# Kernel optimization log

Hardware: AMD Instinct MI355X
Metric: run time of the kernel (lower is better)

Reference implementation:

```python
import jax, jax.numpy as jnp
import numpy as np

N_NODES = 50000
N_EDGES = 800000
IN_FEAT = 128
HEADS = 4
UNITS = 16
LEAKY_ALPHA = 0.2  # tf.nn.leaky_relu default


def setup_inputs() -> dict:
    key = jax.random.key(0)
    k1, k2, k3, k4, k5 = jax.random.split(key, 5)
    x = jax.random.normal(k1, (N_NODES, IN_FEAT), dtype=jnp.float32)
    edge_index = jax.random.randint(k2, (N_EDGES, 2), 0, N_NODES, dtype=jnp.int32)
    # Dense kernel (glorot-ish scaling), no bias (use_bias=False)
    W = jax.random.normal(k3, (IN_FEAT, HEADS * UNITS), dtype=jnp.float32) * (1.0 / np.sqrt(IN_FEAT))
    glorot = np.sqrt(2.0 / (1 + UNITS)).astype(np.float32)
    att_w1 = jax.random.normal(k4, (HEADS, 1, UNITS), dtype=jnp.float32) * glorot
    att_w2 = jax.random.normal(k5, (HEADS, 1, UNITS), dtype=jnp.float32) * glorot
    return {"x": x, "edge_index": edge_index, "W": W, "att_w1": att_w1, "att_w2": att_w2}


def reference(x, edge_index, W, att_w1, att_w2):
    n_nodes = x.shape[0]
    h = x @ W  # [N, H*U]
    snd_idx = edge_index[:, 0]
    rcv_idx = edge_index[:, 1]
    # gather per-edge features, split into heads -> [H, E, U]
    sender = h[snd_idx].reshape(-1, HEADS, UNITS).transpose(1, 0, 2)
    receiver = h[rcv_idx].reshape(-1, HEADS, UNITS).transpose(1, 0, 2)
    # per-edge, per-head attention logits [H, E]
    att = jnp.sum(att_w1 * sender, axis=-1) + jnp.sum(att_w2 * receiver, axis=-1)
    att = jnp.where(att > 0, att, LEAKY_ALPHA * att)
    # segment softmax over receiver neighborhoods, per head
    seg_max = jax.vmap(lambda a: jax.ops.segment_max(a, rcv_idx, num_segments=n_nodes))(att)  # [H, N]
    e = jnp.exp(att - seg_max[:, rcv_idx])
    denom = jax.vmap(lambda a: jax.ops.segment_sum(a, rcv_idx, num_segments=n_nodes))(e)  # [H, N]
    alpha = e / denom[:, rcv_idx]  # [H, E]
    # weighted scatter-sum of sender features -> [H, N, U]
    out = jax.vmap(lambda v: jax.ops.segment_sum(v, rcv_idx, num_segments=n_nodes))(sender * alpha[:, :, None])
    # concat heads -> [N, H*U]; activation is None (identity)
    return out.transpose(1, 0, 2).reshape(n_nodes, HEADS * UNITS)
```

## Files before the change

### kernel.cpp

```cpp
#include <hip/hip_runtime.h>
#include <math.h>

#define N_NODES 50000
#define N_EDGES 800000
#define IN_FEAT 128
#define HEADS   4
#define UNITS   16
#define OUTF    64
#define LEAKY   0.2f

#define NB      196
#define BCAP    5120
#define GEMM_BLKS 782
#define A_BLOCKS  391
#define EPB     8

typedef __attribute__((ext_vector_type(8))) short bf16x8;
typedef __attribute__((ext_vector_type(4))) float f32x4;

__device__ __forceinline__ unsigned short f2bf(float f) {
    unsigned u = __float_as_uint(f);
    unsigned r = u + 0x7FFFu + ((u >> 16) & 1u);
    return (unsigned short)(r >> 16);
}

union SharedU {
    struct { unsigned short xl[64 * 136]; unsigned short wt[64 * 136]; } g;
    struct { int2 stage[2048]; int hist[256], s[256], excl[256],
             gbase[256], cur[256]; } a;
};

__global__ __launch_bounds__(256) void fused_gemm_bucketA(const float* __restrict__ x,
                                                          const float* __restrict__ W,
                                                          const float* __restrict__ w1,
                                                          const float* __restrict__ w2,
                                                          const int2* __restrict__ ei,
                                                          unsigned short* __restrict__ hg,
                                                          float* __restrict__ a1,
                                                          float* __restrict__ a2,
                                                          int* __restrict__ bucket_cnt,
                                                          int2* __restrict__ buckets) {
    __shared__ SharedU sh;
    const int t = threadIdx.x;

    if (blockIdx.x >= GEMM_BLKS) {
        const int e0 = (blockIdx.x - GEMM_BLKS) * 2048;
        sh.a.hist[t] = 0;
        __syncthreads();

        int2 ed[EPB]; int bk[EPB];
        #pragma unroll
        for (int j = 0; j < EPB; ++j) {
            int e = e0 + t + j * 256;
            if (e < N_EDGES) {
                ed[j] = ei[e];
                bk[j] = ed[j].y >> 8;
                atomicAdd(&sh.a.hist[bk[j]], 1);
            } else bk[j] = -1;
        }
        __syncthreads();
        int v = sh.a.hist[t];
        sh.a.s[t] = v;
        __syncthreads();
        #pragma unroll
        for (int off = 1; off < 256; off <<= 1) {
            int u = (t >= off) ? sh.a.s[t - off] : 0;
            __syncthreads();
            sh.a.s[t] += u;
            __syncthreads();
        }
        sh.a.excl[t] = sh.a.s[t] - v;
        sh.a.cur[t] = 0;
        if (t < NB) sh.a.gbase[t] = atomicAdd(&bucket_cnt[t], v);
        __syncthreads();
        #pragma unroll
        for (int j = 0; j < EPB; ++j) {
            if (bk[j] >= 0) {
                int p = sh.a.excl[bk[j]] + atomicAdd(&sh.a.cur[bk[j]], 1);
                sh.a.stage[p] = ed[j];
            }
        }
        __syncthreads();
        const int total = min(2048, N_EDGES - e0);
        for (int i = t; i < total; i += 256) {
            int2 vv = sh.a.stage[i];
            int b = vv.y >> 8;
            buckets[(size_t)b * BCAP + sh.a.gbase[b] + (i - sh.a.excl[b])] = vv;
        }
        return;
    }

    const int node0 = blockIdx.x * 64;
    unsigned short* xl = sh.g.xl;
    unsigned short* wt = sh.g.wt;

    #pragma unroll
    for (int it = 0; it < 8; ++it) {
        int idx = t + 256 * it;
        int r = idx >> 5, q = idx & 31;
        int node = node0 + r;
        float4 v = make_float4(0.f, 0.f, 0.f, 0.f);
        if (node < N_NODES) v = *(const float4*)(x + (size_t)node * IN_FEAT + q * 4);
        ushort4 b;
        b.x = f2bf(v.x); b.y = f2bf(v.y); b.z = f2bf(v.z); b.w = f2bf(v.w);
        *(ushort4*)&xl[r * 136 + q * 4] = b;
    }
    {
        const float4* W4 = (const float4*)W;
        #pragma unroll
        for (int it = 0; it < 8; ++it) {
            int idx4 = t + 256 * it;
            float4 v = W4[idx4];
            int flat = idx4 * 4;
            int k = flat >> 6, c = flat & 63;
            wt[(c + 0) * 136 + k] = f2bf(v.x);
            wt[(c + 1) * 136 + k] = f2bf(v.y);
            wt[(c + 2) * 136 + k] = f2bf(v.z);
            wt[(c + 3) * 136 + k] = f2bf(v.w);
        }
    }
    __syncthreads();

    const int lane = t & 63, wv = t >> 6;
    const int m = lane & 15, quad = lane >> 4;
    const int n0 = wv * 16;

    f32x4 acc[4] = {{0,0,0,0},{0,0,0,0},{0,0,0,0},{0,0,0,0}};
    #pragma unroll
    for (int kc = 0; kc < 4; ++kc) {
        bf16x8 af = *(bf16x8*)&xl[(n0 + m) * 136 + kc * 32 + quad * 8];
        #pragma unroll
        for (int ct = 0; ct < 4; ++ct) {
            bf16x8 bfr = *(bf16x8*)&wt[(ct * 16 + m) * 136 + kc * 32 + quad * 8];
            acc[ct] = __builtin_amdgcn_mfma_f32_16x16x32_bf16(af, bfr, acc[ct], 0, 0, 0);
        }
    }

    #pragma unroll
    for (int ct = 0; ct < 4; ++ct) {
        const float u1 = w1[ct * 16 + m];
        const float u2 = w2[ct * 16 + m];
        #pragma unroll
        for (int r = 0; r < 4; ++r) {
            float p1 = acc[ct][r] * u1;
            float p2 = acc[ct][r] * u2;
            p1 += __shfl_xor(p1, 1, 64); p1 += __shfl_xor(p1, 2, 64);
            p1 += __shfl_xor(p1, 4, 64); p1 += __shfl_xor(p1, 8, 64);
            p2 += __shfl_xor(p2, 1, 64); p2 += __shfl_xor(p2, 2, 64);
            p2 += __shfl_xor(p2, 4, 64); p2 += __shfl_xor(p2, 8, 64);
            if (m == 0) {
                int node = node0 + n0 + quad * 4 + r;
                if (node < N_NODES) {
                    a1[node * 4 + ct] = p1;
                    a2[node * 4 + ct] = p2;
                }
            }
        }
    }

    __syncthreads();
    unsigned short* hl = sh.g.xl;
    #pragma unroll
    for (int ct = 0; ct < 4; ++ct)
        #pragma unroll
        for (int r = 0; r < 4; ++r)
            hl[(n0 + quad * 4 + r) * 72 + ct * 16 + m] = f2bf(acc[ct][r]);
    __syncthreads();
    #pragma unroll
    for (int it = 0; it < 2; ++it) {
        int u = t + 256 * it;
        int r = u >> 3, cg = u & 7;
        int node = node0 + r;
        if (node < N_NODES)
            *(uint4*)&hg[(size_t)node * OUTF + cg * 8] = *(uint4*)&hl[r * 72 + cg * 8];
    }
}

__global__ __launch_bounds__(1024) void bucketB(const int2* __restrict__ buckets,
                                                const int* __restrict__ bucket_cnt,
                                                const float* __restrict__ a1,
                                                const float* __restrict__ a2,
                                                int* __restrict__ edge_snd,
                                                float* __restrict__ edge_e,
                                                int* __restrict__ rs,
                                                int* __restrict__ re) {
    __shared__ int hist[256], cur[256], s[256];
    __shared__ int2 stage[BCAP];
    const int b = blockIdx.x;
    const int t = threadIdx.x;
    const int cnt = bucket_cnt[b];
    if (t < 256) hist[t] = 0;
    __syncthreads();
    for (int i = t; i < cnt; i += 1024) {
        int2 vv = buckets[(size_t)b * BCAP + i];
        stage[i] = vv;
        atomicAdd(&hist[vv.y & 255], 1);
    }
    __syncthreads();
    if (t < 256) s[t] = hist[t];
    __syncthreads();
    #pragma unroll
    for (int off = 1; off < 256; off <<= 1) {
        int u = (t < 256 && t >= off) ? s[t - off] : 0;
        __syncthreads();
        if (t < 256) s[t] += u;
        __syncthreads();
    }
    if (t < 256) {
        const int v = hist[t];
        const int excl = s[t] - v;
        cur[t] = excl;
        const int node = b * 256 + t;
        if (node < N_NODES) {
            rs[node] = b * BCAP + excl;
            re[node] = b * BCAP + excl + v;
        }
    }
    __syncthreads();
    for (int i = t; i < cnt; i += 1024) {
        int2 vv = stage[i];
        int p = atomicAdd(&cur[vv.y & 255], 1);
        float4 s1 = *(const float4*)(a1 + (size_t)vv.x * 4);
        float4 s2 = *(const float4*)(a2 + (size_t)vv.y * 4);
        float t0 = s1.x + s2.x; t0 = t0 > 0.f ? t0 : LEAKY * t0;
        float t1 = s1.y + s2.y; t1 = t1 > 0.f ? t1 : LEAKY * t1;
        float t2 = s1.z + s2.z; t2 = t2 > 0.f ? t2 : LEAKY * t2;
        float t3 = s1.w + s2.w; t3 = t3 > 0.f ? t3 : LEAKY * t3;
        float4 e4 = make_float4(__expf(t0), __expf(t1), __expf(t2), __expf(t3));
        size_t q = (size_t)b * BCAP + p;
        edge_snd[q] = vv.x;
        *(float4*)(edge_e + q * 4) = e4;
    }
}

__global__ __launch_bounds__(256, 8) void gather_kernel(const int* __restrict__ rs,
                                                        const int* __restrict__ re,
                                                        const int* __restrict__ edge_snd,
                                                        const float* __restrict__ edge_e,
                                                        const unsigned short* __restrict__ h,
                                                        float* __restrict__ out) {
    const int wave = threadIdx.x >> 6;
    const int lane = threadIdx.x & 63;
    const int n = blockIdx.x * 4 + wave;
    if (n >= N_NODES) return;
    const int sub  = lane >> 3;
    const int li   = lane & 7;
    const int head = li >> 1;
    const int base = rs[n];
    const int end  = re[n];
    if (end <= base) {
        if (sub == 0) {
            *(float4*)(out + (size_t)n * OUTF + li * 8)     = make_float4(0.f, 0.f, 0.f, 0.f);
            *(float4*)(out + (size_t)n * OUTF + li * 8 + 4) = make_float4(0.f, 0.f, 0.f, 0.f);
        }
        return;
    }
    const uint4* h4 = (const uint4*)h;

    float acc[8] = {0.f,0.f,0.f,0.f,0.f,0.f,0.f,0.f};
    float den = 0.f;

    for (int i = base; i < end; i += 16) {
        #pragma unroll
        for (int g = 0; g < 2; ++g) {
            int eraw = i + g * 8 + sub;
            int eidx = min(eraw, end - 1);
            int s = edge_snd[eidx];
            float ev = edge_e[(size_t)eidx * 4 + head];
            float e = (eraw < end) ? ev : 0.f;
            uint4 hv = h4[(unsigned)(s * 8 + li)];
            const unsigned hw[4] = {hv.x, hv.y, hv.z, hv.w};
            #pragma unroll
            for (int q = 0; q < 4; ++q) {
                acc[q*2+0] = fmaf(e, __uint_as_float(hw[q] << 16),         acc[q*2+0]);
                acc[q*2+1] = fmaf(e, __uint_as_float(hw[q] & 0xFFFF0000u), acc[q*2+1]);
            }
            den += e;
        }
    }

    #pragma unroll
    for (int off = 8; off <= 32; off <<= 1) {
        #pragma unroll
        for (int q = 0; q < 8; ++q) acc[q] += __shfl_xor(acc[q], off, 64);
        den += __shfl_xor(den, off, 64);
    }

    if (sub == 0) {
        float inv = 1.f / den;
        *(float4*)(out + (size_t)n * OUTF + li * 8) =
            make_float4(acc[0] * inv, acc[1] * inv, acc[2] * inv, acc[3] * inv);
        *(float4*)(out + (size_t)n * OUTF + li * 8 + 4) =
            make_float4(acc[4] * inv, acc[5] * inv, acc[6] * inv, acc[7] * inv);
    }
}

extern "C" void kernel_launch(void* const* d_in, const int* in_sizes, int n_in,
                              void* d_out, int out_size, void* d_ws, size_t ws_size,
                              hipStream_t stream) {
    const float* x  = (const float*)d_in[0];
    const int2*  ei = (const int2*)d_in[1];
    const float* W  = (const float*)d_in[2];
    const float* w1 = (const float*)d_in[3];
    const float* w2 = (const float*)d_in[4];
    float* out = (float*)d_out;

    unsigned short* h = (unsigned short*)d_ws;
    float* a1         = (float*)(h + (size_t)N_NODES * OUTF);
    float* a2         = a1 + (size_t)N_NODES * HEADS;
    int2*  buckets    = (int2*)(a2 + (size_t)N_NODES * HEADS);
    float* edge_e     = (float*)(buckets + (size_t)NB * BCAP);
    int*   edge_snd   = (int*)(edge_e + (size_t)NB * BCAP * 4);
    int*   rs         = edge_snd + (size_t)NB * BCAP;
    int*   re         = rs + N_NODES;
    int*   bucket_cnt = re + N_NODES;

    hipMemsetAsync(bucket_cnt, 0, NB * sizeof(int), stream);
    fused_gemm_bucketA<<<GEMM_BLKS + A_BLOCKS, 256, 0, stream>>>(x, W, w1, w2, ei,
                                                                 h, a1, a2,
                                                                 bucket_cnt, buckets);
    bucketB<<<NB, 1024, 0, stream>>>(buckets, bucket_cnt, a1, a2,
                                     edge_snd, edge_e, rs, re);
    gather_kernel<<<(N_NODES + 3) / 4, 256, 0, stream>>>(rs, re, edge_snd, edge_e, h, out);
}
```

Measured before the change: 136.5 us.

## Fuse bucket sort and gather into one kernel with 64-node buckets

Shrinks receiver buckets from 256 to 64 nodes (784 buckets) and merges the second bucketing pass with the gather/aggregation kernel. Sender indices are sorted per node in shared memory and consumed directly. Attention exponentials are recomputed during the gather instead of being written to and read back from global memory, which also removes the edge_snd, edge_e, rs and re buffers and one kernel launch. The tradeoff is fewer, larger blocks in the fused kernel, where each wave walks 16 nodes serially, which may reduce parallelism and load balance. Skewed buckets also risk overflowing the smaller capacity of 1280.

```diff
diff --git a/kernel.cpp b/kernel.cpp
--- a/kernel.cpp
+++ b/kernel.cpp
@@ -9,8 +9,11 @@
 #define OUTF    64
 #define LEAKY   0.2f
 
-#define NB      196
-#define BCAP    5120
+#define BSH     6
+#define BNODES  64
+#define NB      784
+#define NBP     1024
+#define BCAP    1280
 #define GEMM_BLKS 782
 #define A_BLOCKS  391
 #define EPB     8
@@ -26,8 +29,7 @@
 
 union SharedU {
     struct { unsigned short xl[64 * 136]; unsigned short wt[64 * 136]; } g;
-    struct { int2 stage[2048]; int hist[256], s[256], excl[256],
-             gbase[256], cur[256]; } a;
+    struct { int2 stage[2048]; int hist[NBP], cur[NBP], adj[NBP], s[256]; } a;
 };
 
 __global__ __launch_bounds__(256) void fused_gemm_bucketA(const float* __restrict__ x,
@@ -45,7 +47,8 @@
 
     if (blockIdx.x >= GEMM_BLKS) {
         const int e0 = (blockIdx.x - GEMM_BLKS) * 2048;
-        sh.a.hist[t] = 0;
+        #pragma unroll
+        for (int j = 0; j < 4; ++j) sh.a.hist[t + 256 * j] = 0;
         __syncthreads();
 
         int2 ed[EPB]; int bk[EPB];
@@ -54,13 +57,15 @@
             int e = e0 + t + j * 256;
             if (e < N_EDGES) {
                 ed[j] = ei[e];
-                bk[j] = ed[j].y >> 8;
+                bk[j] = ed[j].y >> BSH;
                 atomicAdd(&sh.a.hist[bk[j]], 1);
             } else bk[j] = -1;
         }
         __syncthreads();
-        int v = sh.a.hist[t];
-        sh.a.s[t] = v;
+        const int h0 = sh.a.hist[4 * t + 0], h1 = sh.a.hist[4 * t + 1],
+                  h2 = sh.a.hist[4 * t + 2], h3 = sh.a.hist[4 * t + 3];
+        const int lsum = h0 + h1 + h2 + h3;
+        sh.a.s[t] = lsum;
         __syncthreads();
         #pragma unroll
         for (int off = 1; off < 256; off <<= 1) {
@@ -69,14 +74,23 @@
             sh.a.s[t] += u;
             __syncthreads();
         }
-        sh.a.excl[t] = sh.a.s[t] - v;
-        sh.a.cur[t] = 0;
-        if (t < NB) sh.a.gbase[t] = atomicAdd(&bucket_cnt[t], v);
+        const int base = sh.a.s[t] - lsum;
+        const int ex0 = base, ex1 = base + h0, ex2 = base + h0 + h1, ex3 = base + h0 + h1 + h2;
+        sh.a.cur[4 * t + 0] = ex0; sh.a.cur[4 * t + 1] = ex1;
+        sh.a.cur[4 * t + 2] = ex2; sh.a.cur[4 * t + 3] = ex3;
+        if (4 * t < NB) {
+            int g0 = atomicAdd(&bucket_cnt[4 * t + 0], h0);
+            int g1 = atomicAdd(&bucket_cnt[4 * t + 1], h1);
+            int g2 = atomicAdd(&bucket_cnt[4 * t + 2], h2);
+            int g3 = atomicAdd(&bucket_cnt[4 * t + 3], h3);
+            sh.a.adj[4 * t + 0] = g0 - ex0; sh.a.adj[4 * t + 1] = g1 - ex1;
+            sh.a.adj[4 * t + 2] = g2 - ex2; sh.a.adj[4 * t + 3] = g3 - ex3;
+        }
         __syncthreads();
         #pragma unroll
         for (int j = 0; j < EPB; ++j) {
             if (bk[j] >= 0) {
-                int p = sh.a.excl[bk[j]] + atomicAdd(&sh.a.cur[bk[j]], 1);
+                int p = atomicAdd(&sh.a.cur[bk[j]], 1);
                 sh.a.stage[p] = ed[j];
             }
         }
@@ -84,8 +98,8 @@
         const int total = min(2048, N_EDGES - e0);
         for (int i = t; i < total; i += 256) {
             int2 vv = sh.a.stage[i];
-            int b = vv.y >> 8;
-            buckets[(size_t)b * BCAP + sh.a.gbase[b] + (i - sh.a.excl[b])] = vv;
+            int b = vv.y >> BSH;
+            buckets[(size_t)(b * BCAP + sh.a.adj[b] + i)] = vv;
         }
         return;
     }
@@ -176,122 +190,103 @@
     }
 }
 
-__global__ __launch_bounds__(1024) void bucketB(const int2* __restrict__ buckets,
+__global__ __launch_bounds__(256) void bucketBC(const int2* __restrict__ buckets,
                                                 const int* __restrict__ bucket_cnt,
                                                 const float* __restrict__ a1,
                                                 const float* __restrict__ a2,
-                                                int* __restrict__ edge_snd,
-                                                float* __restrict__ edge_e,
-                                                int* __restrict__ rs,
-                                                int* __restrict__ re) {
-    __shared__ int hist[256], cur[256], s[256];
+                                                const unsigned short* __restrict__ h,
+                                                float* __restrict__ out) {
     __shared__ int2 stage[BCAP];
+    __shared__ int  snds[BCAP];
+    __shared__ int  hist[BNODES], strt[BNODES], cur[BNODES];
     const int b = blockIdx.x;
     const int t = threadIdx.x;
     const int cnt = bucket_cnt[b];
-    if (t < 256) hist[t] = 0;
-    __syncthreads();
-    for (int i = t; i < cnt; i += 1024) {
+
+    if (t < BNODES) hist[t] = 0;
+    __syncthreads();
+    for (int i = t; i < cnt; i += 256) {
         int2 vv = buckets[(size_t)b * BCAP + i];
         stage[i] = vv;
-        atomicAdd(&hist[vv.y & 255], 1);
-    }
-    __syncthreads();
-    if (t < 256) s[t] = hist[t];
-    __syncthreads();
-    #pragma unroll
-    for (int off = 1; off < 256; off <<= 1) {
-        int u = (t < 256 && t >= off) ? s[t - off] : 0;
-        __syncthreads();
-        if (t < 256) s[t] += u;
-        __syncthreads();
-    }
-    if (t < 256) {
-        const int v = hist[t];
-        const int excl = s[t] - v;
-        cur[t] = excl;
-        const int node = b * 256 + t;
-        if (node < N_NODES) {
-            rs[node] = b * BCAP + excl;
-            re[node] = b * BCAP + excl + v;
-        }
-    }
-    __syncthreads();
-    for (int i = t; i < cnt; i += 1024) {
+        atomicAdd(&hist[vv.y & (BNODES - 1)], 1);
+    }
+    __syncthreads();
+    if (t < 64) {
+        int v = hist[t];
+        int inc = v;
+        #pragma unroll
+        for (int off = 1; off < 64; off <<= 1) {
+            int u = __shfl_up(inc, off, 64);
+            if (t >= off) inc += u;
+        }
+        strt[t] = inc - v;
+        cur[t]  = inc - v;
+    }
+    __syncthreads();
+    for (int i = t; i < cnt; i += 256) {
         int2 vv = stage[i];
-        int p = atomicAdd(&cur[vv.y & 255], 1);
-        float4 s1 = *(const float4*)(a1 + (size_t)vv.x * 4);
-        float4 s2 = *(const float4*)(a2 + (size_t)vv.y * 4);
-        float t0 = s1.x + s2.x; t0 = t0 > 0.f ? t0 : LEAKY * t0;
-        float t1 = s1.y + s2.y; t1 = t1 > 0.f ? t1 : LEAKY * t1;
-        float t2 = s1.z + s2.z; t2 = t2 > 0.f ? t2 : LEAKY * t2;
-        float t3 = s1.w + s2.w; t3 = t3 > 0.f ? t3 : LEAKY * t3;
-        float4 e4 = make_float4(__expf(t0), __expf(t1), __expf(t2), __expf(t3));
-        size_t q = (size_t)b * BCAP + p;
-        edge_snd[q] = vv.x;
-        *(float4*)(edge_e + q * 4) = e4;
-    }
-}
-
-__global__ __launch_bounds__(256, 8) void gather_kernel(const int* __restrict__ rs,
-                                                        const int* __restrict__ re,
-                                                        const int* __restrict__ edge_snd,
-                                                        const float* __restrict__ edge_e,
-                                                        const unsigned short* __restrict__ h,
-                                                        float* __restrict__ out) {
-    const int wave = threadIdx.x >> 6;
-    const int lane = threadIdx.x & 63;
-    const int n = blockIdx.x * 4 + wave;
-    if (n >= N_NODES) return;
+        int p = atomicAdd(&cur[vv.y & (BNODES - 1)], 1);
+        snds[p] = vv.x;
+    }
+    __syncthreads();
+
+    const int lane = t & 63, wv = t >> 6;
     const int sub  = lane >> 3;
     const int li   = lane & 7;
     const int head = li >> 1;
-    const int base = rs[n];
-    const int end  = re[n];
-    if (end <= base) {
+    const uint4* h4 = (const uint4*)h;
+
+    for (int j = 0; j < 16; ++j) {
+        const int loc  = wv + j * 4;
+        const int node = b * BNODES + loc;
+        if (node >= N_NODES) break;
+        const int s0 = strt[loc];
+        const int cn = hist[loc];
+        if (cn == 0) {
+            if (sub == 0) {
+                *(float4*)(out + (size_t)node * OUTF + li * 8)     = make_float4(0.f, 0.f, 0.f, 0.f);
+                *(float4*)(out + (size_t)node * OUTF + li * 8 + 4) = make_float4(0.f, 0.f, 0.f, 0.f);
+            }
+            continue;
+        }
+        const float a2h = a2[node * 4 + head];
+        float acc[8] = {0.f,0.f,0.f,0.f,0.f,0.f,0.f,0.f};
+        float den = 0.f;
+
+        for (int i0 = 0; i0 < cn; i0 += 16) {
+            #pragma unroll
+            for (int g = 0; g < 2; ++g) {
+                int er = i0 + g * 8 + sub;
+                int ec = min(er, cn - 1);
+                int s = snds[s0 + ec];
+                float t0 = a1[s * 4 + head] + a2h;
+                t0 = t0 > 0.f ? t0 : LEAKY * t0;
+                float e = (er < cn) ? __expf(t0) : 0.f;
+                uint4 hv = h4[(unsigned)(s * 8 + li)];
+                const unsigned hw[4] = {hv.x, hv.y, hv.z, hv.w};
+                #pragma unroll
+                for (int q = 0; q < 4; ++q) {
+                    acc[q*2+0] = fmaf(e, __uint_as_float(hw[q] << 16),         acc[q*2+0]);
+                    acc[q*2+1] = fmaf(e, __uint_as_float(hw[q] & 0xFFFF0000u), acc[q*2+1]);
+                }
+                den += e;
+            }
+        }
+
+        #pragma unroll
+        for (int off = 8; off <= 32; off <<= 1) {
+            #pragma unroll
+            for (int q = 0; q < 8; ++q) acc[q] += __shfl_xor(acc[q], off, 64);
+            den += __shfl_xor(den, off, 64);
+        }
+
         if (sub == 0) {
-            *(float4*)(out + (size_t)n * OUTF + li * 8)     = make_float4(0.f, 0.f, 0.f, 0.f);
-            *(float4*)(out + (size_t)n * OUTF + li * 8 + 4) = make_float4(0.f, 0.f, 0.f, 0.f);
-        }
-        return;
-    }
-    const uint4* h4 = (const uint4*)h;
-
-    float acc[8] = {0.f,0.f,0.f,0.f,0.f,0.f,0.f,0.f};
-    float den = 0.f;
-
-    for (int i = base; i < end; i += 16) {
-        #pragma unroll
-        for (int g = 0; g < 2; ++g) {
-            int eraw = i + g * 8 + sub;
-            int eidx = min(eraw, end - 1);
-            int s = edge_snd[eidx];
-            float ev = edge_e[(size_t)eidx * 4 + head];
-            float e = (eraw < end) ? ev : 0.f;
-            uint4 hv = h4[(unsigned)(s * 8 + li)];
-            const unsigned hw[4] = {hv.x, hv.y, hv.z, hv.w};
-            #pragma unroll
-            for (int q = 0; q < 4; ++q) {
-                acc[q*2+0] = fmaf(e, __uint_as_float(hw[q] << 16),         acc[q*2+0]);
-                acc[q*2+1] = fmaf(e, __uint_as_float(hw[q] & 0xFFFF0000u), acc[q*2+1]);
-            }
-            den += e;
-        }
-    }
-
-    #pragma unroll
-    for (int off = 8; off <= 32; off <<= 1) {
-        #pragma unroll
-        for (int q = 0; q < 8; ++q) acc[q] += __shfl_xor(acc[q], off, 64);
-        den += __shfl_xor(den, off, 64);
-    }
-
-    if (sub == 0) {
-        float inv = 1.f / den;
-        *(float4*)(out + (size_t)n * OUTF + li * 8) =
-            make_float4(acc[0] * inv, acc[1] * inv, acc[2] * inv, acc[3] * inv);
-        *(float4*)(out + (size_t)n * OUTF + li * 8 + 4) =
-            make_float4(acc[4] * inv, acc[5] * inv, acc[6] * inv, acc[7] * inv);
+            float inv = 1.f / den;
+            *(float4*)(out + (size_t)node * OUTF + li * 8) =
+                make_float4(acc[0] * inv, acc[1] * inv, acc[2] * inv, acc[3] * inv);
+            *(float4*)(out + (size_t)node * OUTF + li * 8 + 4) =
+                make_float4(acc[4] * inv, acc[5] * inv, acc[6] * inv, acc[7] * inv);
+        }
     }
 }
 
@@ -309,17 +304,11 @@
     float* a1         = (float*)(h + (size_t)N_NODES * OUTF);
     float* a2         = a1 + (size_t)N_NODES * HEADS;
     int2*  buckets    = (int2*)(a2 + (size_t)N_NODES * HEADS);
-    float* edge_e     = (float*)(buckets + (size_t)NB * BCAP);
-    int*   edge_snd   = (int*)(edge_e + (size_t)NB * BCAP * 4);
-    int*   rs         = edge_snd + (size_t)NB * BCAP;
-    int*   re         = rs + N_NODES;
-    int*   bucket_cnt = re + N_NODES;
+    int*   bucket_cnt = (int*)(buckets + (size_t)NB * BCAP);
 
     hipMemsetAsync(bucket_cnt, 0, NB * sizeof(int), stream);
     fused_gemm_bucketA<<<GEMM_BLKS + A_BLOCKS, 256, 0, stream>>>(x, W, w1, w2, ei,
                                                                  h, a1, a2,
                                                                  bucket_cnt, buckets);
-    bucketB<<<NB, 1024, 0, stream>>>(buckets, bucket_cnt, a1, a2,
-                                     edge_snd, edge_e, rs, re);
-    gather_kernel<<<(N_NODES + 3) / 4, 256, 0, stream>>>(rs, re, edge_snd, edge_e, h, out);
+    bucketBC<<<NB, 256, 0, stream>>>(buckets, bucket_cnt, a1, a2, h, out);
 }
```

Result: slower. 160.1 us (+17.3%).
